# Performance work log

Hardware: AMD Instinct MI355X
Metric: run time of the kernel (lower is better)

## Reference

```python
import jax, jax.numpy as jnp
import numpy as np

MAX_N = 21
COORD = 3
TOTAL_T = 100
K_RANK = 3
POWER_STEPS = 10


def _recon_single(D, Wt, u_noise, x_noise):
    """D, Wt: [N,N]; u_noise: [K_RANK,N]; x_noise: [N,3]. Returns X: [N,3]."""
    N = MAX_N
    # dist_to_gram (classical MDS double-centering)
    D_row = jnp.sum(D, 0, keepdims=True) / N
    D_col = jnp.sum(D, 1, keepdims=True) / N
    D_mean = jnp.sum(D) / (N * N)
    B = -0.5 * (D - D_row - D_col + D_mean)
    # low_rank_approx_power: k=3 deflated power iterations, 10 steps each
    A = B
    us = []
    for i in range(K_RANK):
        u = u_noise[i]
        for _ in range(POWER_STEPS):
            # F.normalize(u, dim=0, p=2, eps=0.001)
            u = u / jnp.maximum(jnp.linalg.norm(u), 1e-3)
            u = A @ u
        eig_sq = jnp.sum(u * u)
        u = u / jnp.power(eig_sq + 0.01, 0.25)
        us.append(u)
        A = A - jnp.outer(u, u)
    X0 = jnp.stack(us, -1) + x_noise  # [N,3]

    T = jnp.float32(TOTAL_T)

    def energy(X):
        diff = X[None, :, :] - X[:, None, :]          # [N,N,3], D_X[i,j]=||X_j-X_i||^2
        D_X = jnp.sum(diff * diff, -1) + 0.01
        return jnp.sum(Wt * jnp.square(D - D_X))

    def step(X, t):
        g = jax.grad(energy)(X)
        dX = -0.1 * g
        speed = jnp.sqrt(jnp.sum(dX * dX, 1, keepdims=True) + 1e-3)
        alpha_t = 0.1 + (5.0 - 0.1) * ((T - t) / T)
        scale = alpha_t * jnp.tanh(speed / alpha_t) / speed
        return X + dX * scale, None

    X, _ = jax.lax.scan(step, X0, jnp.arange(TOTAL_T, dtype=jnp.float32))
    return X


def _forward(gnn_edge_out, W1, b1, W2, b2, u_noise, x_noise, batch_size):
    h_nf = W1.shape[1]
    # edge_mlp1 (MLP with 1 layer -> Linear + ReLU)
    edge_out = jax.nn.relu(gnn_edge_out @ W1 + b1)                     # [B*N*N, h]
    emb = jnp.sum(edge_out.reshape(batch_size, MAX_N, MAX_N, h_nf), axis=(1, 2))  # [B, h]
    # edge_mlp2 -> symmetrize -> softplus
    e2 = (edge_out @ W2 + b2).reshape(batch_size, MAX_N, MAX_N, 2)
    e2 = e2 + jnp.transpose(e2, (0, 2, 1, 3))
    dw = jax.nn.softplus(e2)
    D_init = dw[..., 0] * (1.0 - jnp.eye(MAX_N, dtype=dw.dtype))       # [B,N,N]
    W = dw[..., 1]                                                     # [B,N,N]
    X_pred = jax.vmap(_recon_single)(D_init, W, u_noise, x_noise)      # [B,N,3]
    return D_init, W, emb, X_pred


def setup_inputs() -> dict:
    key = jax.random.key(0)
    ks = jax.random.split(key, 5)
    B, h_nf = 1024, 256
    n_edges = B * MAX_N * MAX_N
    return {
        "gnn_edge_out": jax.random.normal(ks[0], (n_edges, h_nf), jnp.float32),
        "W1": jax.random.normal(ks[1], (h_nf, h_nf), jnp.float32) * (1.0 / np.sqrt(h_nf)),
        "b1": jnp.zeros((h_nf,), jnp.float32),
        "W2": jax.random.normal(ks[2], (h_nf, 2), jnp.float32) * (1.0 / np.sqrt(h_nf)),
        "b2": jnp.zeros((2,), jnp.float32),
        "u_noise": jax.random.normal(ks[3], (B, K_RANK, MAX_N), jnp.float32),
        "x_noise": jax.random.normal(ks[4], (B, MAX_N, COORD), jnp.float32),
        "batch_size": B,
    }


def reference(gnn_edge_out, W1, b1, W2, b2, u_noise, x_noise, batch_size):
    return _forward(gnn_edge_out, W1, b1, W2, b2, u_noise, x_noise, batch_size)
```

## Files before the change

kernel.cpp:

```cpp
#include <hip/hip_runtime.h>
#include <hip/hip_bf16.h>
#include <math.h>

#define B_SZ 1024
#define NMAX 21
#define NN 441
#define HNF 256
#define TOT_ROWS (B_SZ * NN)
#define TILES_PER_BATCH 7
#define BMV 63

typedef short short8 __attribute__((ext_vector_type(8)));
typedef float float4v __attribute__((ext_vector_type(4)));

__device__ __forceinline__ float softplus_f(float x) {
    return fmaxf(x, 0.f) + log1pf(expf(-fabsf(x)));
}

__device__ __forceinline__ unsigned short f2bf(float x) {
    union { float f; unsigned int u; } v; v.f = x;
    unsigned int r = v.u + 0x7FFFu + ((v.u >> 16) & 1u);
    return (unsigned short)(r >> 16);
}

__device__ __forceinline__ unsigned pk_bf16(float lo, float hi) {
    __hip_bfloat162 h = __float22bfloat162_rn(float2{lo, hi});
    return *reinterpret_cast<unsigned*>(&h);
}

__device__ __forceinline__ float bcast(float v, int q) {
    int i = __builtin_amdgcn_readlane(__builtin_bit_cast(int, v), q);
    return __builtin_bit_cast(float, i);
}

__device__ __forceinline__ float tanh_fast(float x) {
    float e = __builtin_amdgcn_exp2f(x * 2.8853900817779268f);
    float q = __builtin_amdgcn_rcpf(e + 1.f);
    return fmaf(-2.f, q, 1.f);
}

__global__ __launch_bounds__(256) void pack_w1(const float* __restrict__ W1,
                                               short* __restrict__ B0p,
                                               float* __restrict__ emb)
{
    int id = blockIdx.x * 256 + threadIdx.x;
    int j = id & 7, l = (id >> 3) & 63, f = (id >> 9) & 15, s = id >> 13;
    int k = s * 32 + ((l >> 4) << 3) + j;
    int c = (f << 4) + (l & 15);
    B0p[id] = (short)f2bf(W1[k * HNF + c]);
    #pragma unroll
    for (int e = 0; e < 4; e++)
        emb[(size_t)e * 65536 + id] = 0.f;
}

__global__ __launch_bounds__(512, 4) void fused_mlp_bf16(
    const float* __restrict__ gnn, const short* __restrict__ B0p,
    const float* __restrict__ b1, const float* __restrict__ W2,
    const float* __restrict__ b2,
    float* __restrict__ Dreg, float* __restrict__ Wreg, float* __restrict__ emb)
{
    __shared__ __align__(16) char ldsbuf[65536];
    float* stage = (float*)ldsbuf;
    short* Abf   = (short*)ldsbuf;
    __shared__ float red0[8][64];
    __shared__ float red1[8][64];

    const int t = threadIdx.x;
    const int w = t >> 6, l = t & 63;
    const int batch = blockIdx.x / TILES_PER_BATCH;
    const int tile  = blockIdx.x % TILES_PER_BATCH;
    const long row0 = (long)batch * NN + (long)tile * BMV;

    #pragma unroll
    for (int i = 0; i < 8; i++) {
        int r = (w << 3) + i;
        long ar = row0 + r;
        if (ar >= (long)TOT_ROWS) ar = TOT_ROWS - 1;
        int j = (l & 56) | ((l ^ (l >> 3) ^ r) & 7);
        const float* gsrc = gnn + ar * HNF + (j << 2);
        __builtin_amdgcn_global_load_lds(
            (const __attribute__((address_space(1))) unsigned*)gsrc,
            (__attribute__((address_space(3))) unsigned*)(stage + (r << 8)),
            16, 0, 0);
    }
    __syncthreads();

    const int r = t >> 3, c = t & 7;
    float4 fr[8];
    #pragma unroll
    for (int i = 0; i < 8; i++) {
        int pc = (c << 3) | ((i ^ c ^ r) & 7);
        fr[i] = *(const float4*)(stage + (r << 8) + (pc << 2));
    }
    __syncthreads();
    {
        const int mr = r >> 4;
        #pragma unroll
        for (int g = 0; g < 4; g++) {
            uint4 pv;
            pv.x = pk_bf16(fr[2*g].x,   fr[2*g].y);
            pv.y = pk_bf16(fr[2*g].z,   fr[2*g].w);
            pv.z = pk_bf16(fr[2*g+1].x, fr[2*g+1].y);
            pv.w = pk_bf16(fr[2*g+1].z, fr[2*g+1].w);
            int di = (((c << 2) + mr) << 6) + (g << 4) + (r & 15);
            *(uint4*)(Abf + ((size_t)(di ^ c) << 3)) = pv;
        }
    }
    __syncthreads();

    const int frow = l & 15;
    const int fk   = l >> 4;

    float4v acc[4][2];
    #pragma unroll
    for (int m = 0; m < 4; m++)
        #pragma unroll
        for (int n = 0; n < 2; n++)
            acc[m][n] = (float4v){0.f, 0.f, 0.f, 0.f};

    #pragma unroll 2
    for (int kk = 0; kk < 8; ++kk) {
        short8 bf[2], af[4];
        #pragma unroll
        for (int n = 0; n < 2; n++) {
            int nf = (w << 1) + n;
            size_t off = (size_t)((((kk << 4) + nf) << 6) | l) << 3;
            bf[n] = *(const short8*)(B0p + off);
        }
        #pragma unroll
        for (int m = 0; m < 4; m++) {
            int di = ((((kk << 2) + m) << 6) | l) ^ kk;
            af[m] = *(const short8*)(Abf + (size_t)di * 8);
        }
        #pragma unroll
        for (int m = 0; m < 4; m++)
            #pragma unroll
            for (int n = 0; n < 2; n++)
                acc[m][n] = __builtin_amdgcn_mfma_f32_16x16x32_bf16(af[m], bf[n], acc[m][n], 0, 0, 0);
    }

    float w20[2], w21[2], b1v[2];
    #pragma unroll
    for (int n = 0; n < 2; n++) {
        int cc = (((w << 1) + n) << 4) + frow;
        b1v[n] = b1[cc];
        w20[n] = W2[2 * cc];
        w21[n] = W2[2 * cc + 1];
    }
    float ps0[4][4], ps1[4][4], embp[2] = {0.f, 0.f};
    #pragma unroll
    for (int m = 0; m < 4; m++)
        #pragma unroll
        for (int j = 0; j < 4; j++) { ps0[m][j] = 0.f; ps1[m][j] = 0.f; }

    #pragma unroll
    for (int m = 0; m < 4; m++)
        #pragma unroll
        for (int n = 0; n < 2; n++)
            #pragma unroll
            for (int j = 0; j < 4; j++) {
                float h = fmaxf(acc[m][n][j] + b1v[n], 0.f);
                ps0[m][j] += h * w20[n];
                ps1[m][j] += h * w21[n];
                int row = (m << 4) + (fk << 2) + j;
                if (row < BMV) embp[n] += h;
            }

    #pragma unroll
    for (int off = 1; off < 16; off <<= 1)
        #pragma unroll
        for (int m = 0; m < 4; m++)
            #pragma unroll
            for (int j = 0; j < 4; j++) {
                ps0[m][j] += __shfl_xor(ps0[m][j], off);
                ps1[m][j] += __shfl_xor(ps1[m][j], off);
            }
    if (frow == 0) {
        #pragma unroll
        for (int m = 0; m < 4; m++)
            #pragma unroll
            for (int j = 0; j < 4; j++) {
                int row = (m << 4) + (fk << 2) + j;
                red0[w][row] = ps0[m][j];
                red1[w][row] = ps1[m][j];
            }
    }

    #pragma unroll
    for (int n = 0; n < 2; n++) {
        embp[n] += __shfl_xor(embp[n], 16);
        embp[n] += __shfl_xor(embp[n], 32);
    }
    if (l < 16) {
        #pragma unroll
        for (int n = 0; n < 2; n++)
            atomicAdd(emb + (size_t)batch * 256 + (((w << 1) + n) << 4) + l, embp[n]);
    }

    __syncthreads();
    if (t < BMV) {
        float v0 = b2[0], v1 = b2[1];
        #pragma unroll
        for (int ww = 0; ww < 8; ww++) { v0 += red0[ww][t]; v1 += red1[ww][t]; }
        Dreg[row0 + t] = v0;
        Wreg[row0 + t] = v1;
    }
}

__global__ __launch_bounds__(64) void symrecon_kernel(
    float* __restrict__ Dreg, float* __restrict__ Wreg,
    const float* __restrict__ un, const float* __restrict__ xn,
    float* __restrict__ Xo)
{
    const int b = blockIdx.x, l = threadIdx.x;
    __shared__ float R0[NN], R1[NN];

    float* Db = Dreg + (size_t)b * NN;
    float* Wb = Wreg + (size_t)b * NN;
    for (int idx = l; idx < NN; idx += 64) { R0[idx] = Db[idx]; R1[idx] = Wb[idx]; }
    __syncthreads();

    const bool act = (l < NMAX);
    const int li = act ? l : 0;
    float Drow[NMAX], Wrow[NMAX], WD[NMAX];
    float rs = 0.f;
    #pragma unroll
    for (int q = 0; q < NMAX; q++) {
        float rd = R0[li * NMAX + q] + R0[q * NMAX + li];
        float rw = R1[li * NMAX + q] + R1[q * NMAX + li];
        float d = (q == li) ? 0.f : softplus_f(rd);
        float wv = softplus_f(rw);
        Drow[q] = act ? d : 0.f;
        Wrow[q] = act ? wv : 0.f;
        WD[q] = Wrow[q] * Drow[q];
        rs += Drow[q];
    }
    if (act) {
        #pragma unroll
        for (int q = 0; q < NMAX; q++) {
            Db[l * NMAX + q] = Drow[q];
            Wb[l * NMAX + q] = Wrow[q];
        }
    }

    float tot = rs;
    #pragma unroll
    for (int m = 1; m < 32; m <<= 1) tot += __shfl_xor(tot, m);
    const float mean = tot * (1.f / (float)NN);
    const float rsn = rs * (1.f / (float)NMAX);
    float Arow[NMAX];
    #pragma unroll
    for (int q = 0; q < NMAX; q++) {
        float rsq = bcast(rsn, q);
        float v = -0.5f * (Drow[q] - rsn - rsq + mean);
        Arow[q] = act ? v : 0.f;
    }

    float xr[3] = {0.f, 0.f, 0.f};
    #pragma unroll
    for (int e = 0; e < 3; e++) {
        float u = act ? un[(size_t)b * 63 + e * NMAX + l] : 0.f;
        for (int s = 0; s < 10; s++) {
            float n2 = u * u;
            #pragma unroll
            for (int m = 1; m < 32; m <<= 1) n2 += __shfl_xor(n2, m);
            u *= fminf(__builtin_amdgcn_rsqf(n2), 1000.f);
            float a0 = 0.f, a1 = 0.f, a2 = 0.f;
            #pragma unroll
            for (int q = 0; q < NMAX; q++) {
                float uq = bcast(u, q);
                if ((q % 3) == 0)      a0 = fmaf(Arow[q], uq, a0);
                else if ((q % 3) == 1) a1 = fmaf(Arow[q], uq, a1);
                else                   a2 = fmaf(Arow[q], uq, a2);
            }
            u = act ? ((a0 + a1) + a2) : 0.f;
        }
        float e2 = u * u;
        #pragma unroll
        for (int m = 1; m < 32; m <<= 1) e2 += __shfl_xor(e2, m);
        u *= sqrtf(__builtin_amdgcn_rsqf(e2 + 0.01f));
        xr[e] = u;
        #pragma unroll
        for (int q = 0; q < NMAX; q++) Arow[q] = fmaf(-u, bcast(u, q), Arow[q]);
    }
    float x = xr[0], y = xr[1], z = xr[2];
    if (act) {
        x += xn[(size_t)b * 63 + l * 3 + 0];
        y += xn[(size_t)b * 63 + l * 3 + 1];
        z += xn[(size_t)b * 63 + l * 3 + 2];
    }

    for (int tstep = 0; tstep < 100; tstep++) {
        float gx0=0.f,gx1=0.f,gx2=0.f, gy0=0.f,gy1=0.f,gy2=0.f,
              gz0=0.f,gz1=0.f,gz2=0.f;
        #pragma unroll
        for (int q = 0; q < NMAX; q++) {
            float dx = x - bcast(x, q);
            float dy = y - bcast(y, q);
            float dz = z - bcast(z, q);
            float s = fmaf(dx, dx, fmaf(dy, dy, fmaf(dz, dz, 0.01f)));
            float cm = fmaf(-Wrow[q], s, WD[q]);
            if ((q % 3) == 0)      { gx0 = fmaf(cm,dx,gx0); gy0 = fmaf(cm,dy,gy0); gz0 = fmaf(cm,dz,gz0); }
            else if ((q % 3) == 1) { gx1 = fmaf(cm,dx,gx1); gy1 = fmaf(cm,dy,gy1); gz1 = fmaf(cm,dz,gz1); }
            else                   { gx2 = fmaf(cm,dx,gx2); gy2 = fmaf(cm,dy,gy2); gz2 = fmaf(cm,dz,gz2); }
        }
        float d0 = 0.8f * ((gx0 + gx1) + gx2);
        float d1 = 0.8f * ((gy0 + gy1) + gy2);
        float d2 = 0.8f * ((gz0 + gz1) + gz2);
        float ss = fmaf(d0, d0, fmaf(d1, d1, fmaf(d2, d2, 1e-3f)));
        float inv_sp = __builtin_amdgcn_rsqf(ss);
        float speed  = ss * inv_sp;
        float alpha  = fmaf(-0.049f, (float)tstep, 5.0f);
        float th     = tanh_fast(speed * __builtin_amdgcn_rcpf(alpha));
        float scale  = alpha * th * inv_sp;
        x = fmaf(d0, scale, x);
        y = fmaf(d1, scale, y);
        z = fmaf(d2, scale, z);
    }
    if (act) {
        Xo[(size_t)b * 63 + l * 3 + 0] = x;
        Xo[(size_t)b * 63 + l * 3 + 1] = y;
        Xo[(size_t)b * 63 + l * 3 + 2] = z;
    }
}

extern "C" void kernel_launch(void* const* d_in, const int* in_sizes, int n_in,
                              void* d_out, int out_size, void* d_ws, size_t ws_size,
                              hipStream_t stream) {
    const float* gnn = (const float*)d_in[0];
    const float* W1  = (const float*)d_in[1];
    const float* b1  = (const float*)d_in[2];
    const float* W2  = (const float*)d_in[3];
    const float* b2  = (const float*)d_in[4];
    const float* un  = (const float*)d_in[5];
    const float* xn  = (const float*)d_in[6];

    float* out  = (float*)d_out;
    float* Dreg = out;
    float* Wreg = out + (size_t)TOT_ROWS;
    float* emb  = out + (size_t)2 * TOT_ROWS;
    float* Xo   = out + (size_t)2 * TOT_ROWS + B_SZ*256;

    short* B0p = (short*)d_ws;

    pack_w1<<<dim3(256), dim3(256), 0, stream>>>(W1, B0p, emb);

    fused_mlp_bf16<<<dim3(B_SZ * TILES_PER_BATCH), dim3(512), 0, stream>>>(
        gnn, B0p, b1, W2, b2, Dreg, Wreg, emb);

    symrecon_kernel<<<dim3(B_SZ), dim3(64), 0, stream>>>(Dreg, Wreg, un, xn, Xo);
}
```

Baseline: 292.1 us.

## Split recon columns across both wave halves and broadcast via LDS

The per-batch reconstruction kernel now has the two 32-lane halves of its 64-lane wave each handle 11 of the 21 columns. Partial sums are combined with a cross-half shuffle, and lanes 32-63 are no longer idle. Values that were broadcast with readlane (row sums, power-iteration vectors, coordinates) are now shared through small LDS arrays. Softplus is replaced by an exp2/log hardware-intrinsic approximation. This shortens the serial per-step dependency chain in the power iterations and the 100 gradient steps, at the cost of extra LDS traffic and shuffles. Correctness without barriers relies on the block being a single wavefront.

```diff
diff --git a/kernel.cpp b/kernel.cpp
--- a/kernel.cpp
+++ b/kernel.cpp
@@ -13,10 +13,6 @@
 typedef short short8 __attribute__((ext_vector_type(8)));
 typedef float float4v __attribute__((ext_vector_type(4)));
 
-__device__ __forceinline__ float softplus_f(float x) {
-    return fmaxf(x, 0.f) + log1pf(expf(-fabsf(x)));
-}
-
 __device__ __forceinline__ unsigned short f2bf(float x) {
     union { float f; unsigned int u; } v; v.f = x;
     unsigned int r = v.u + 0x7FFFu + ((v.u >> 16) & 1u);
@@ -28,9 +24,10 @@
     return *reinterpret_cast<unsigned*>(&h);
 }
 
-__device__ __forceinline__ float bcast(float v, int q) {
-    int i = __builtin_amdgcn_readlane(__builtin_bit_cast(int, v), q);
-    return __builtin_bit_cast(float, i);
+__device__ __forceinline__ float softplus_fast(float x) {
+    float e = __builtin_amdgcn_exp2f(-fabsf(x) * 1.44269504088896f);
+    float lg = __builtin_amdgcn_logf(1.f + e);
+    return fmaxf(x, 0.f) + 0.69314718055995f * lg;
 }
 
 __device__ __forceinline__ float tanh_fast(float x) {
@@ -214,99 +211,112 @@
 {
     const int b = blockIdx.x, l = threadIdx.x;
     __shared__ float R0[NN], R1[NN];
+    __shared__ float Rs[22], Us[22], Xs[3][22];
 
     float* Db = Dreg + (size_t)b * NN;
     float* Wb = Wreg + (size_t)b * NN;
     for (int idx = l; idx < NN; idx += 64) { R0[idx] = Db[idx]; R1[idx] = Wb[idx]; }
-    __syncthreads();
-
-    const bool act = (l < NMAX);
-    const int li = act ? l : 0;
-    float Drow[NMAX], Wrow[NMAX], WD[NMAX];
-    float rs = 0.f;
-    #pragma unroll
-    for (int q = 0; q < NMAX; q++) {
-        float rd = R0[li * NMAX + q] + R0[q * NMAX + li];
-        float rw = R1[li * NMAX + q] + R1[q * NMAX + li];
-        float d = (q == li) ? 0.f : softplus_f(rd);
-        float wv = softplus_f(rw);
-        Drow[q] = act ? d : 0.f;
-        Wrow[q] = act ? wv : 0.f;
-        WD[q] = Wrow[q] * Drow[q];
-        rs += Drow[q];
+    if (l == 0) { Rs[21] = 0.f; Us[21] = 0.f; Xs[0][21] = 0.f; Xs[1][21] = 0.f; Xs[2][21] = 0.f; }
+    __syncthreads();
+
+    const int half = l >> 5;
+    const int li   = l & 31;
+    const bool act = li < NMAX;
+    const int li0  = act ? li : 0;
+    const int q0   = half * 11;
+
+    float Drow[11], Wrow[11], WD[11];
+    float rsh = 0.f;
+    #pragma unroll
+    for (int j = 0; j < 11; j++) {
+        int q = q0 + j;
+        bool v = act && (q < NMAX);
+        int qc = v ? q : 0;
+        float rd = R0[li0 * NMAX + qc] + R0[qc * NMAX + li0];
+        float rw = R1[li0 * NMAX + qc] + R1[qc * NMAX + li0];
+        float d  = (v && q != li) ? softplus_fast(rd) : 0.f;
+        float wv = v ? softplus_fast(rw) : 0.f;
+        Drow[j] = d; Wrow[j] = wv; WD[j] = wv * d;
+        rsh += d;
     }
     if (act) {
         #pragma unroll
-        for (int q = 0; q < NMAX; q++) {
-            Db[l * NMAX + q] = Drow[q];
-            Wb[l * NMAX + q] = Wrow[q];
-        }
-    }
-
-    float tot = rs;
-    #pragma unroll
-    for (int m = 1; m < 32; m <<= 1) tot += __shfl_xor(tot, m);
+        for (int j = 0; j < 11; j++) {
+            int q = q0 + j;
+            if (q < NMAX) {
+                Db[li * NMAX + q] = Drow[j];
+                Wb[li * NMAX + q] = Wrow[j];
+            }
+        }
+    }
+
+    float rsf = rsh + __shfl_xor(rsh, 32);
+    float tot = rsh;
+    #pragma unroll
+    for (int m = 1; m < 64; m <<= 1) tot += __shfl_xor(tot, m);
     const float mean = tot * (1.f / (float)NN);
-    const float rsn = rs * (1.f / (float)NMAX);
-    float Arow[NMAX];
-    #pragma unroll
-    for (int q = 0; q < NMAX; q++) {
-        float rsq = bcast(rsn, q);
-        float v = -0.5f * (Drow[q] - rsn - rsq + mean);
-        Arow[q] = act ? v : 0.f;
-    }
-
-    float xr[3] = {0.f, 0.f, 0.f};
+    const float rsn  = rsf * (1.f / (float)NMAX);
+    if (act && half == 0) Rs[li] = rsn;
+    float Arow[11];
+    #pragma unroll
+    for (int j = 0; j < 11; j++) {
+        int q = q0 + j;
+        bool v = act && (q < NMAX);
+        float rsq = Rs[q];
+        Arow[j] = v ? -0.5f * (Drow[j] - rsn - rsq + mean) : 0.f;
+    }
+
+    float xc[3];
     #pragma unroll
     for (int e = 0; e < 3; e++) {
-        float u = act ? un[(size_t)b * 63 + e * NMAX + l] : 0.f;
+        float u = act ? un[(size_t)b * 63 + e * NMAX + li] : 0.f;
         for (int s = 0; s < 10; s++) {
-            float n2 = u * u;
-            #pragma unroll
-            for (int m = 1; m < 32; m <<= 1) n2 += __shfl_xor(n2, m);
+            float n2 = (act && half == 0) ? u * u : 0.f;
+            #pragma unroll
+            for (int m = 1; m < 64; m <<= 1) n2 += __shfl_xor(n2, m);
             u *= fminf(__builtin_amdgcn_rsqf(n2), 1000.f);
-            float a0 = 0.f, a1 = 0.f, a2 = 0.f;
-            #pragma unroll
-            for (int q = 0; q < NMAX; q++) {
-                float uq = bcast(u, q);
-                if ((q % 3) == 0)      a0 = fmaf(Arow[q], uq, a0);
-                else if ((q % 3) == 1) a1 = fmaf(Arow[q], uq, a1);
-                else                   a2 = fmaf(Arow[q], uq, a2);
-            }
-            u = act ? ((a0 + a1) + a2) : 0.f;
-        }
-        float e2 = u * u;
-        #pragma unroll
-        for (int m = 1; m < 32; m <<= 1) e2 += __shfl_xor(e2, m);
+            if (act && half == 0) Us[li] = u;
+            float a = 0.f;
+            #pragma unroll
+            for (int j = 0; j < 11; j++) a = fmaf(Arow[j], Us[q0 + j], a);
+            a += __shfl_xor(a, 32);
+            u = act ? a : 0.f;
+        }
+        float e2 = (act && half == 0) ? u * u : 0.f;
+        #pragma unroll
+        for (int m = 1; m < 64; m <<= 1) e2 += __shfl_xor(e2, m);
         u *= sqrtf(__builtin_amdgcn_rsqf(e2 + 0.01f));
-        xr[e] = u;
-        #pragma unroll
-        for (int q = 0; q < NMAX; q++) Arow[q] = fmaf(-u, bcast(u, q), Arow[q]);
-    }
-    float x = xr[0], y = xr[1], z = xr[2];
+        xc[e] = u;
+        if (act && half == 0) Us[li] = u;
+        #pragma unroll
+        for (int j = 0; j < 11; j++) Arow[j] = fmaf(-u, Us[q0 + j], Arow[j]);
+    }
+    float x = xc[0], y = xc[1], z = xc[2];
     if (act) {
-        x += xn[(size_t)b * 63 + l * 3 + 0];
-        y += xn[(size_t)b * 63 + l * 3 + 1];
-        z += xn[(size_t)b * 63 + l * 3 + 2];
-    }
+        x += xn[(size_t)b * 63 + li * 3 + 0];
+        y += xn[(size_t)b * 63 + li * 3 + 1];
+        z += xn[(size_t)b * 63 + li * 3 + 2];
+    }
+    if (act && half == 0) { Xs[0][li] = x; Xs[1][li] = y; Xs[2][li] = z; }
 
     for (int tstep = 0; tstep < 100; tstep++) {
-        float gx0=0.f,gx1=0.f,gx2=0.f, gy0=0.f,gy1=0.f,gy2=0.f,
-              gz0=0.f,gz1=0.f,gz2=0.f;
-        #pragma unroll
-        for (int q = 0; q < NMAX; q++) {
-            float dx = x - bcast(x, q);
-            float dy = y - bcast(y, q);
-            float dz = z - bcast(z, q);
-            float s = fmaf(dx, dx, fmaf(dy, dy, fmaf(dz, dz, 0.01f)));
-            float cm = fmaf(-Wrow[q], s, WD[q]);
-            if ((q % 3) == 0)      { gx0 = fmaf(cm,dx,gx0); gy0 = fmaf(cm,dy,gy0); gz0 = fmaf(cm,dz,gz0); }
-            else if ((q % 3) == 1) { gx1 = fmaf(cm,dx,gx1); gy1 = fmaf(cm,dy,gy1); gz1 = fmaf(cm,dz,gz1); }
-            else                   { gx2 = fmaf(cm,dx,gx2); gy2 = fmaf(cm,dy,gy2); gz2 = fmaf(cm,dz,gz2); }
-        }
-        float d0 = 0.8f * ((gx0 + gx1) + gx2);
-        float d1 = 0.8f * ((gy0 + gy1) + gy2);
-        float d2 = 0.8f * ((gz0 + gz1) + gz2);
+        float gx = 0.f, gy = 0.f, gz = 0.f;
+        #pragma unroll
+        for (int j = 0; j < 11; j++) {
+            int q = q0 + j;
+            float dx = x - Xs[0][q];
+            float dy = y - Xs[1][q];
+            float dz = z - Xs[2][q];
+            float s  = fmaf(dx, dx, fmaf(dy, dy, fmaf(dz, dz, 0.01f)));
+            float cm = fmaf(-Wrow[j], s, WD[j]);
+            gx = fmaf(cm, dx, gx);
+            gy = fmaf(cm, dy, gy);
+            gz = fmaf(cm, dz, gz);
+        }
+        gx += __shfl_xor(gx, 32);
+        gy += __shfl_xor(gy, 32);
+        gz += __shfl_xor(gz, 32);
+        float d0 = 0.8f * gx, d1 = 0.8f * gy, d2 = 0.8f * gz;
         float ss = fmaf(d0, d0, fmaf(d1, d1, fmaf(d2, d2, 1e-3f)));
         float inv_sp = __builtin_amdgcn_rsqf(ss);
         float speed  = ss * inv_sp;
@@ -316,11 +326,12 @@
         x = fmaf(d0, scale, x);
         y = fmaf(d1, scale, y);
         z = fmaf(d2, scale, z);
-    }
-    if (act) {
-        Xo[(size_t)b * 63 + l * 3 + 0] = x;
-        Xo[(size_t)b * 63 + l * 3 + 1] = y;
-        Xo[(size_t)b * 63 + l * 3 + 2] = z;
+        if (act && half == 0) { Xs[0][li] = x; Xs[1][li] = y; Xs[2][li] = z; }
+    }
+    if (act && half == 0) {
+        Xo[(size_t)b * 63 + li * 3 + 0] = x;
+        Xo[(size_t)b * 63 + li * 3 + 1] = y;
+        Xo[(size_t)b * 63 + li * 3 + 2] = z;
     }
 }
 
```

Result: faster. 267.1 us (-8.5%).
